# Kernel optimization log

Hardware: AMD Instinct MI355X
Metric: run time of the kernel (lower is better)

## Reference

```python
import math
import jax, jax.numpy as jnp
import numpy as np

# Frozen random shifts from the original module's __init__ (random.randint(-1,1))
SHIFT_C = 1   # p_2_0_1: roll along channel dim
SHIFT_H = 1   # p_4_1_0: roll along h
SHIFT_W = -1  # p_4_1_1: roll along w
K = 7         # horizontal window size (F.unfold kernel (1,7), padding (0,3))


def setup_inputs() -> dict:
    key = jax.random.key(0)
    k1, k2 = jax.random.split(key)
    n, c, h, w = 8, 256, 56, 56
    x = jax.random.normal(k1, (n, c, h, w), dtype=jnp.float32)
    # p_1_w ~ trunc_normal(std=0.1) around 1.0; approximate with 1 + 0.1*normal
    p1w = 1.0 + 0.1 * jax.random.normal(k2, (1, c, h, w), dtype=jnp.float32)
    return {"x": x, "p1w": p1w}


def _unfold_w7(t):
    # t: (n,c,h,w) -> (n,c,7,h,w): 7 horizontal taps, zero-padded (pad=3)
    w = t.shape[-1]
    tp = jnp.pad(t, ((0, 0), (0, 0), (0, 0), (3, 3)))
    return jnp.stack([tp[..., j:j + w] for j in range(K)], axis=2)


def reference(x, p1w):
    n, c, h, w = x.shape
    hw = h * w
    t1 = p1w * x                              # (n,c,h,w)
    t2 = jnp.roll(t1, SHIFT_C, axis=1)        # roll channels
    t3 = _unfold_w7(t2)                       # (n,c,7,h,w)
    t4 = jnp.roll(jnp.roll(t3, SHIFT_H, axis=3), SHIFT_W, axis=4)
    t5 = t1[:, :, None] - t3                  # (n,c,7,h,w)
    t6 = x[:, :, None] + t4                   # (n,c,7,h,w)
    x2 = x.reshape(n, c, hw)
    t5r = t5.reshape(n, c, K, hw)
    t6r = t6.reshape(n, c, K, hw)
    # scores: bmm(x (n,c,hw), t5^T (n,hw,c*7)) -> (n,c,c,7)
    t7 = jnp.einsum('nip,njkp->nijk', x2, t5r) / math.sqrt(hw)
    # aggregate: bmm(t7 (n,c,c*7), t6 (n,c*7,hw)) -> (n,c,hw)
    t8 = jnp.einsum('nijk,njkp->nip', t7, t6r) / math.sqrt(c * K)
    return t8.reshape(n, c, h, w)
```

## Files before the change

kernel.cpp:

```cpp
#include <hip/hip_runtime.h>

typedef unsigned short u16;
typedef unsigned int u32;
typedef unsigned long long u64;
typedef __bf16 bf16x8 __attribute__((ext_vector_type(8)));
typedef float f32x4 __attribute__((ext_vector_type(4)));

#define HH  56
#define WW  56
#define HW  3136
#define CC  256
#define NB  8
#define CKP 2048
#define KS1 4

__device__ __forceinline__ u16 f2bf(float f) {
  unsigned int u = __float_as_uint(f);
  u += 0x7fffu + ((u >> 16) & 1u);
  return (u16)(u >> 16);
}
__device__ __forceinline__ float bf2f(u16 v) {
  return __uint_as_float((unsigned)v << 16);
}

__device__ __forceinline__ void lds_load16(const void* g, void* l) {
  __builtin_amdgcn_global_load_lds(
      (const __attribute__((address_space(1))) void*)g,
      (__attribute__((address_space(3))) void*)l, 16, 0, 0);
}

__global__ void pass1(const float* __restrict__ x, const float* __restrict__ p1w,
                      u16* __restrict__ t1b, u16* __restrict__ xb) {
  const int bi = blockIdx.x;
  const int nb = bi & 7;
  const int inner = bi >> 3;
  const int cw = inner * 256 + threadIdx.x;
  const int i  = nb * (CC * HW / 4) + cw;
  float4 xv = ((const float4*)x)[i];
  float4 wv = ((const float4*)p1w)[cw];
  uint2 xo = make_uint2((unsigned)f2bf(xv.x) | ((unsigned)f2bf(xv.y) << 16),
                        (unsigned)f2bf(xv.z) | ((unsigned)f2bf(xv.w) << 16));
  ((uint2*)xb)[i] = xo;
  uint2 to = make_uint2((unsigned)f2bf(xv.x * wv.x) | ((unsigned)f2bf(xv.y * wv.y) << 16),
                        (unsigned)f2bf(xv.z * wv.z) | ((unsigned)f2bf(xv.w * wv.w) << 16));
  ((uint2*)t1b)[i] = to;
}

__global__ __launch_bounds__(256)
void gemm1f(const u16* __restrict__ A, const u16* __restrict__ t1b,
            float* __restrict__ Cp) {
  __shared__ u16 As[128 * 64];
  __shared__ u16 Bs[128 * 64];

  const int bi = blockIdx.x;
  const int nb = bi & 7;
  const int r  = bi >> 3;
  const int ks = r & 3;
  const int r2 = r >> 2;
  const int m0b = r2 & 1;
  const int n0b = r2 >> 1;

  const int it0 = 49 * ks / KS1, it1 = 49 * (ks + 1) / KS1;
  const u16* Ab  = A   + (long)nb * CC * HW;
  const u16* t1n = t1b + (long)nb * CC * HW;
  const int m0 = m0b * 128, n0 = n0b * 128;
  const int jb = n0b * 16;
  const int t = threadIdx.x;
  const int lane = t & 63, wave = t >> 6;
  const int wm = wave & 1, wn = wave >> 1;
  const int lm = lane & 15, quad = lane >> 4;

  const int jl = (t >> 3) & 15, pc = t & 7, hf = t >> 7;
  const int j  = jb + jl;
  const int jm = (j + CC - 1) & (CC - 1);
  const u16* arow = t1n + (long)j  * HW;
  const u16* wrow = t1n + (long)jm * HW;

  f32x4 acc[4][4];
#pragma unroll
  for (int a = 0; a < 4; ++a)
#pragma unroll
    for (int b = 0; b < 4; ++b) acc[a][b] = (f32x4)0.0f;

  int rowc[4], colc[4];
#pragma unroll
  for (int ci = 0; ci < 4; ++ci) {
    int c = t + ci * 256;
    rowc[ci] = c >> 3;
    colc[ci] = ((c & 7) ^ (rowc[ci] & 7)) * 8;
  }

  for (int it = it0; it < it1; ++it) {
    const int k0 = it * 64;
#pragma unroll
    for (int ci = 0; ci < 4; ++ci)
      lds_load16(Ab + (long)(m0 + rowc[ci]) * HW + k0 + colc[ci],
                 &As[(t + ci * 256) * 8]);

    {
      const int p8 = k0 + pc * 8;
      __attribute__((aligned(16))) u16 Ar[8];
      __attribute__((aligned(16))) u16 Wd[24];
      *(uint4*)Ar = *(const uint4*)&arow[p8];
#pragma unroll
      for (int L = 0; L < 3; ++L) {
        int ad = p8 - 8 + L * 8;
        ad = ad < 0 ? 0 : (ad > HW - 8 ? HW - 8 : ad);
        *(uint4*)&Wd[L * 8] = *(const uint4*)&wrow[ad];
      }
      const int w0t = p8 % 56;
      if (hf == 0) {
#pragma unroll
        for (int k = 0; k < 4; ++k) {
          __attribute__((aligned(16))) u16 v[8];
#pragma unroll
          for (int e = 0; e < 8; ++e)
            v[e] = ((unsigned)(w0t + e + k - 3) < 56u) ? Wd[e + k + 5] : (u16)0;
          *(uint4*)&Bs[(jl * 8 + k) * 64 + (pc ^ k) * 8] = *(const uint4*)v;
        }
      } else {
#pragma unroll
        for (int k = 4; k < 7; ++k) {
          __attribute__((aligned(16))) u16 v[8];
#pragma unroll
          for (int e = 0; e < 8; ++e)
            v[e] = ((unsigned)(w0t + e + k - 3) < 56u) ? Wd[e + k + 5] : (u16)0;
          *(uint4*)&Bs[(jl * 8 + k) * 64 + (pc ^ k) * 8] = *(const uint4*)v;
        }
        *(uint4*)&Bs[(jl * 8 + 7) * 64 + (pc ^ 7) * 8] = *(const uint4*)Ar;
      }
    }
    __syncthreads();
#pragma unroll
    for (int kk = 0; kk < 2; ++kk) {
      const int phys = ((kk * 4 + quad) ^ (lm & 7)) * 8;
      bf16x8 af[4], bv[4];
#pragma unroll
      for (int mi = 0; mi < 4; ++mi)
        af[mi] = *(const bf16x8*)&As[(wm * 64 + mi * 16 + lm) * 64 + phys];
#pragma unroll
      for (int ni = 0; ni < 4; ++ni)
        bv[ni] = *(const bf16x8*)&Bs[(wn * 64 + ni * 16 + lm) * 64 + phys];
#pragma unroll
      for (int mi = 0; mi < 4; ++mi)
#pragma unroll
        for (int ni = 0; ni < 4; ++ni)
          acc[mi][ni] = __builtin_amdgcn_mfma_f32_16x16x32_bf16(
              af[mi], bv[ni], acc[mi][ni], 0, 0, 0);
    }
    __syncthreads();
  }

  float* Cb = Cp + ((long)ks * NB + nb) * (long)CC * CKP;
#pragma unroll
  for (int mi = 0; mi < 4; ++mi)
#pragma unroll
    for (int ni = 0; ni < 4; ++ni) {
      int rb = m0 + wm * 64 + mi * 16 + quad * 4;
      int cg = n0 + wn * 64 + ni * 16 + lm;
#pragma unroll
      for (int r4 = 0; r4 < 4; ++r4)
        Cb[(long)(rb + r4) * CKP + cg] = acc[mi][ni][r4];
    }
}

__global__ void reduce1(const float* __restrict__ p1, u16* __restrict__ t7) {
  const int bi = blockIdx.x;
  const int nb = bi & 7;
  const int gg = (bi >> 3) * 256 + threadIdx.x;
  const long S = (long)NB * CC * CKP;
  const long base = (long)nb * CC * CKP + (long)gg * 8;
  float a[8];
#pragma unroll
  for (int e = 0; e < 8; ++e) a[e] = 0.0f;
#pragma unroll
  for (int ks = 0; ks < KS1; ++ks) {
    float4 lo = *(const float4*)&p1[ks * S + base];
    float4 hi = *(const float4*)&p1[ks * S + base + 4];
    a[0] += lo.x; a[1] += lo.y; a[2] += lo.z; a[3] += lo.w;
    a[4] += hi.x; a[5] += hi.y; a[6] += hi.z; a[7] += hi.w;
  }
  const float s = 1.0f / 56.0f;
  const float G = a[7];
  __attribute__((aligned(16))) u16 o[8];
  float s7 = 0.0f;
#pragma unroll
  for (int k = 0; k < 7; ++k) {
    float v = (G - a[k]) * s;
    s7 += v;
    o[k] = f2bf(v);
  }
  o[7] = f2bf(s7);
  *(uint4*)&t7[base] = *(const uint4*)o;
}

__global__ __launch_bounds__(256)
void gemm2f(const u16* __restrict__ A, const u16* __restrict__ xb,
            const u16* __restrict__ t1b, float* __restrict__ out) {
  __shared__ u16 As0[128 * 64], As1[128 * 64];
  __shared__ u16 Bs[64 * 64];
  __shared__ __attribute__((aligned(16))) u16 Rs0[912], Rs1[912];
  __shared__ __attribute__((aligned(16))) u16 Xs0[512], Xs1[512];

  const int bi = blockIdx.x;
  const int nb = bi & 7;
  const int r  = bi >> 3;
  const int m0b = r & 1;
  const int n0b = r >> 1;

  const u16* Ab  = A   + (long)nb * CC * CKP;
  const u16* xbn = xb  + (long)nb * CC * HW;
  const u16* t1n = t1b + (long)nb * CC * HW;
  const int m0 = m0b * 128, n0 = n0b * 64;
  const int t = threadIdx.x;
  const int lane = t & 63, wave = t >> 6;
  const int wm = wave & 1, wn = wave >> 1;
  const int lm = lane & 15, quad = lane >> 4;

  const int pr = t & 63, jg = t >> 6;
  const int p  = n0 + pr;
  const int h  = p / WW, w = p - h * WW;
  const int w2 = (w + 1) % WW;
  const int swz = pr & 7;
  const int h_lo = n0 / WW;
  const int slot = h - h_lo;

  const int sA   = ((jg * 2 + 0) * 2 + slot) * 56 + w2 - 3;
  const int s4   = sA & ~3;
  const u32 sh   = (u32)(sA & 3) * 16;
  const int b0   = 8 + s4;
  const int b1   = b0 + 112;
  u32 mk01, mk23, mk45, mk6;
  {
    u32 m[7];
#pragma unroll
    for (int k = 0; k < 7; ++k)
      m[k] = ((unsigned)(w2 + k - 3) < 56u) ? 0xffffu : 0u;
    mk01 = m[0] | (m[1] << 16);
    mk23 = m[2] | (m[3] << 16);
    mk45 = m[4] | (m[5] << 16);
    mk6  = m[6];
  }
  const int xoff0 = (jg * 2 + 0) * 64 + pr;
  const int xoff1 = (jg * 2 + 1) * 64 + pr;

  long stSrcOff = 0;
  int  stCh = 0;
  bool stR = false, stX = false;
  {
    if (wave == 1) {
      stX = true; stCh = lane >> 3;
      stSrcOff = n0 + (lane & 7) * 8;
    } else if (wave == 2 || (wave == 3 && lane < 48)) {
      stR = true;
      int c = (wave == 2) ? lane : 64 + lane;
      stCh = c / 14;
      int rem = c - stCh * 14;
      int s = rem / 7, i = rem - s * 7;
      int h2s = ((h_lo + s) + HH - 1) % HH;
      stSrcOff = h2s * 56 + i * 8;
    }
  }

  f32x4 acc[4][2];
#pragma unroll
  for (int a = 0; a < 4; ++a)
#pragma unroll
    for (int b = 0; b < 2; ++b) acc[a][b] = (f32x4)0.0f;

  int rowc[4], colc[4];
#pragma unroll
  for (int ci = 0; ci < 4; ++ci) {
    int c = t + ci * 256;
    rowc[ci] = c >> 3;
    colc[ci] = ((c & 7) ^ (rowc[ci] & 7)) * 8;
  }

#define DMAA(AsD, itn) do { const int k0_ = (itn) * 64;                        \
    _Pragma("unroll")                                                          \
    for (int ci = 0; ci < 4; ++ci)                                             \
      lds_load16(Ab + (long)(m0 + rowc[ci]) * CKP + k0_ + colc[ci],            \
                 &AsD[(t + ci * 256) * 8]); } while (0)

#define STAGE(RsD, XsD, itn) do {                                              \
    if (stX)                                                                   \
      lds_load16(xbn + (long)((itn) * 8 + stCh) * HW + stSrcOff,               \
                 &XsD[lane * 8]);                                              \
    else if (stR) {                                                            \
      const int jmm_ = ((itn) * 8 + stCh + CC - 1) & (CC - 1);                 \
      lds_load16(t1n + (long)jmm_ * HW + stSrcOff,                             \
                 (wave == 2) ? &RsD[8 + lane * 8] : &RsD[8 + 512 + lane * 8]); \
    } } while (0)

#define TAPS(RsS, bofs, xr, d4) do {                                           \
    u64 q0 = *(const u64*)&(RsS)[(bofs)];                                      \
    u64 q1 = *(const u64*)&(RsS)[(bofs) + 4];                                  \
    u64 q2 = *(const u64*)&(RsS)[(bofs) + 8];                                  \
    u64 a_ = (q0 >> sh) | (sh ? (q1 << (64u - sh)) : 0ull);                    \
    u64 b_ = (q1 >> sh) | (sh ? (q2 << (64u - sh)) : 0ull);                    \
    (d4) = make_uint4(((u32)a_) & mk01, ((u32)(a_ >> 32)) & mk23,              \
                      ((u32)b_) & mk45,                                        \
                      (((u32)(b_ >> 32)) & mk6) | ((u32)(xr) << 16));          \
  } while (0)

#define BGEN(RsS, XsS) do {                                                    \
    u16 xr0_ = XsS[xoff0], xr1_ = XsS[xoff1];                                  \
    uint4 d0_, d1_;                                                            \
    TAPS(RsS, b0, xr0_, d0_);                                                  \
    TAPS(RsS, b1, xr1_, d1_);                                                  \
    *(uint4*)&Bs[pr * 64 + (((jg * 2 + 0) ^ swz) * 8)] = d0_;                  \
    *(uint4*)&Bs[pr * 64 + (((jg * 2 + 1) ^ swz) * 8)] = d1_;                  \
  } while (0)

#define MFMA2(AsS) do {                                                        \
    _Pragma("unroll")                                                          \
    for (int kk = 0; kk < 2; ++kk) {                                           \
      const int phys = ((kk * 4 + quad) ^ (lm & 7)) * 8;                       \
      bf16x8 af[4], bv[2];                                                     \
      _Pragma("unroll")                                                        \
      for (int mi = 0; mi < 4; ++mi)                                           \
        af[mi] = *(const bf16x8*)&(AsS)[(wm * 64 + mi * 16 + lm) * 64 + phys]; \
      _Pragma("unroll")                                                        \
      for (int ni = 0; ni < 2; ++ni)                                           \
        bv[ni] = *(const bf16x8*)&Bs[(wn * 32 + ni * 16 + lm) * 64 + phys];    \
      _Pragma("unroll")                                                        \
      for (int mi = 0; mi < 4; ++mi)                                           \
        _Pragma("unroll")                                                      \
        for (int ni = 0; ni < 2; ++ni)                                         \
          acc[mi][ni] = __builtin_amdgcn_mfma_f32_16x16x32_bf16(               \
              af[mi], bv[ni], acc[mi][ni], 0, 0, 0);                           \
    } } while (0)

  STAGE(Rs0, Xs0, 0);
  DMAA(As0, 0);
  __syncthreads();

  for (int itp = 0; itp < 16; ++itp) {
    const int itE = itp * 2;
    BGEN(Rs0, Xs0);
    __syncthreads();
    DMAA(As1, itE + 1);
    STAGE(Rs1, Xs1, itE + 1);
    MFMA2(As0);
    __syncthreads();
    BGEN(Rs1, Xs1);
    __syncthreads();
    if (itE + 2 < 32) {
      DMAA(As0, itE + 2);
      STAGE(Rs0, Xs0, itE + 2);
    }
    MFMA2(As1);
    __syncthreads();
  }

#undef DMAA
#undef STAGE
#undef TAPS
#undef BGEN
#undef MFMA2

  const float s2 = 0.023622783f;
  float* Ob = out + (long)nb * CC * HW;
#pragma unroll
  for (int mi = 0; mi < 4; ++mi)
#pragma unroll
    for (int ni = 0; ni < 2; ++ni) {
      int rb = m0 + wm * 64 + mi * 16 + quad * 4;
      int cg = n0 + wn * 32 + ni * 16 + lm;
#pragma unroll
      for (int r4 = 0; r4 < 4; ++r4)
        Ob[(long)(rb + r4) * HW + cg] = acc[mi][ni][r4] * s2;
    }
}

extern "C" void kernel_launch(void* const* d_in, const int* in_sizes, int n_in,
                              void* d_out, int out_size, void* d_ws, size_t ws_size,
                              hipStream_t stream) {
  const float* x   = (const float*)d_in[0];
  const float* p1w = (const float*)d_in[1];

  char* ws = (char*)d_ws;
  size_t o = 0;
  u16* xb  = (u16*)(ws + o); o += (size_t)NB * CC * HW * 2;
  u16* t1b = (u16*)(ws + o); o += (size_t)NB * CC * HW * 2;
  u16* t7  = (u16*)(ws + o); o += (size_t)NB * CC * CKP * 2;
  float* p1 = (float*)(ws + o); o += (size_t)KS1 * NB * CC * CKP * 4;

  pass1<<<NB * CC * HW / 4 / 256, 256, 0, stream>>>(x, p1w, t1b, xb);
  gemm1f<<<NB * KS1 * 2 * 16, 256, 0, stream>>>(xb, t1b, p1);
  reduce1<<<NB * CC * CKP / 8 / 256, 256, 0, stream>>>(p1, t7);
  gemm2f<<<NB * 2 * 49, 256, 0, stream>>>(t7, xb, t1b, (float*)d_out);
}
```

Baseline: 181.4 us.

## Warp-specialize gemm2f into producer and MFMA consumer waves with double-buffered B

Splits the four waves of gemm2f into two consumer waves that only run MFMAs (each owning a 64x64 output tile with 4x4 accumulators) and two producer waves that stage A via LDS DMA, build the B tile from t1 taps, and prefetch x values straight from global into registers. B is now double-buffered so producers fill the next buffer while consumers compute on the current one, cutting from four barriers per pair of iterations to two. This aims to overlap B-tile generation and loads with MFMA work. In exchange it halves the waves issuing MFMAs, raises per-consumer register pressure, and replaces the LDS-staged x with uncoalesced-ish scalar global loads.

```diff
diff --git a/kernel.cpp b/kernel.cpp
--- a/kernel.cpp
+++ b/kernel.cpp
@@ -198,9 +198,8 @@
 void gemm2f(const u16* __restrict__ A, const u16* __restrict__ xb,
             const u16* __restrict__ t1b, float* __restrict__ out) {
   __shared__ u16 As0[128 * 64], As1[128 * 64];
-  __shared__ u16 Bs[64 * 64];
+  __shared__ u16 Bs0[64 * 64], Bs1[64 * 64];
   __shared__ __attribute__((aligned(16))) u16 Rs0[912], Rs1[912];
-  __shared__ __attribute__((aligned(16))) u16 Xs0[512], Xs1[512];
 
   const int bi = blockIdx.x;
   const int nb = bi & 7;
@@ -214,10 +213,11 @@
   const int m0 = m0b * 128, n0 = n0b * 64;
   const int t = threadIdx.x;
   const int lane = t & 63, wave = t >> 6;
-  const int wm = wave & 1, wn = wave >> 1;
+  const bool consumer = (wave < 2);
   const int lm = lane & 15, quad = lane >> 4;
 
-  const int pr = t & 63, jg = t >> 6;
+  const int pid = t & 127;
+  const int pr = pid & 63, jgrp = pid >> 6;
   const int p  = n0 + pr;
   const int h  = p / WW, w = p - h * WW;
   const int w2 = (w + 1) % WW;
@@ -225,11 +225,10 @@
   const int h_lo = n0 / WW;
   const int slot = h - h_lo;
 
-  const int sA   = ((jg * 2 + 0) * 2 + slot) * 56 + w2 - 3;
-  const int s4   = sA & ~3;
-  const u32 sh   = (u32)(sA & 3) * 16;
-  const int b0   = 8 + s4;
-  const int b1   = b0 + 112;
+  const int sA0  = slot * 56 + w2 - 3;
+  const int s4   = sA0 & ~3;
+  const u32 sh   = (u32)(sA0 & 3) * 16;
+  const int bb   = 8 + s4;
   u32 mk01, mk23, mk45, mk6;
   {
     u32 m[7];
@@ -241,58 +240,52 @@
     mk45 = m[4] | (m[5] << 16);
     mk6  = m[6];
   }
-  const int xoff0 = (jg * 2 + 0) * 64 + pr;
-  const int xoff1 = (jg * 2 + 1) * 64 + pr;
 
   long stSrcOff = 0;
   int  stCh = 0;
-  bool stR = false, stX = false;
-  {
-    if (wave == 1) {
-      stX = true; stCh = lane >> 3;
-      stSrcOff = n0 + (lane & 7) * 8;
-    } else if (wave == 2 || (wave == 3 && lane < 48)) {
-      stR = true;
-      int c = (wave == 2) ? lane : 64 + lane;
-      stCh = c / 14;
-      int rem = c - stCh * 14;
-      int s = rem / 7, i = rem - s * 7;
-      int h2s = ((h_lo + s) + HH - 1) % HH;
-      stSrcOff = h2s * 56 + i * 8;
-    }
-  }
-
-  f32x4 acc[4][2];
-#pragma unroll
-  for (int a = 0; a < 4; ++a)
-#pragma unroll
-    for (int b = 0; b < 2; ++b) acc[a][b] = (f32x4)0.0f;
-
-  int rowc[4], colc[4];
-#pragma unroll
-  for (int ci = 0; ci < 4; ++ci) {
-    int c = t + ci * 256;
+  const bool stR = (!consumer) && (pid < 112);
+  if (stR) {
+    stCh = pid / 14;
+    int rem = pid - stCh * 14;
+    int s = rem / 7, i = rem - s * 7;
+    int h2s = ((h_lo + s) + HH - 1) % HH;
+    stSrcOff = h2s * 56 + i * 8;
+  }
+
+  int rowc[8], colc[8];
+#pragma unroll
+  for (int ci = 0; ci < 8; ++ci) {
+    int c = pid + ci * 128;
     rowc[ci] = c >> 3;
     colc[ci] = ((c & 7) ^ (rowc[ci] & 7)) * 8;
   }
 
+  f32x4 acc[4][4];
+#pragma unroll
+  for (int a = 0; a < 4; ++a)
+#pragma unroll
+    for (int b = 0; b < 4; ++b) acc[a][b] = (f32x4)0.0f;
+
+  u16 xrE[4], xrO[4];
+
 #define DMAA(AsD, itn) do { const int k0_ = (itn) * 64;                        \
     _Pragma("unroll")                                                          \
-    for (int ci = 0; ci < 4; ++ci)                                             \
+    for (int ci = 0; ci < 8; ++ci)                                             \
       lds_load16(Ab + (long)(m0 + rowc[ci]) * CKP + k0_ + colc[ci],            \
-                 &AsD[(t + ci * 256) * 8]); } while (0)
-
-#define STAGE(RsD, XsD, itn) do {                                              \
-    if (stX)                                                                   \
-      lds_load16(xbn + (long)((itn) * 8 + stCh) * HW + stSrcOff,               \
-                 &XsD[lane * 8]);                                              \
-    else if (stR) {                                                            \
-      const int jmm_ = ((itn) * 8 + stCh + CC - 1) & (CC - 1);                 \
-      lds_load16(t1n + (long)jmm_ * HW + stSrcOff,                             \
-                 (wave == 2) ? &RsD[8 + lane * 8] : &RsD[8 + 512 + lane * 8]); \
-    } } while (0)
-
-#define TAPS(RsS, bofs, xr, d4) do {                                           \
+                 &AsD[(pid + ci * 128) * 8]); } while (0)
+
+#define STAGER(RsD, itn) do { if (stR) {                                       \
+    const int jmm_ = ((itn) * 8 + stCh + CC - 1) & (CC - 1);                   \
+    lds_load16(t1n + (long)jmm_ * HW + stSrcOff,                               \
+               (wave == 2) ? &RsD[8 + lane * 8] : &RsD[8 + 512 + lane * 8]);   \
+  } } while (0)
+
+#define XPF(xr, itn) do {                                                      \
+    _Pragma("unroll")                                                          \
+    for (int cc = 0; cc < 4; ++cc)                                             \
+      (xr)[cc] = xbn[(long)((itn) * 8 + jgrp * 4 + cc) * HW + p]; } while (0)
+
+#define TAPS(RsS, bofs, xr1, d4) do {                                          \
     u64 q0 = *(const u64*)&(RsS)[(bofs)];                                      \
     u64 q1 = *(const u64*)&(RsS)[(bofs) + 4];                                  \
     u64 q2 = *(const u64*)&(RsS)[(bofs) + 8];                                  \
@@ -300,77 +293,91 @@
     u64 b_ = (q1 >> sh) | (sh ? (q2 << (64u - sh)) : 0ull);                    \
     (d4) = make_uint4(((u32)a_) & mk01, ((u32)(a_ >> 32)) & mk23,              \
                       ((u32)b_) & mk45,                                        \
-                      (((u32)(b_ >> 32)) & mk6) | ((u32)(xr) << 16));          \
+                      (((u32)(b_ >> 32)) & mk6) | ((u32)(xr1) << 16));         \
   } while (0)
 
-#define BGEN(RsS, XsS) do {                                                    \
-    u16 xr0_ = XsS[xoff0], xr1_ = XsS[xoff1];                                  \
-    uint4 d0_, d1_;                                                            \
-    TAPS(RsS, b0, xr0_, d0_);                                                  \
-    TAPS(RsS, b1, xr1_, d1_);                                                  \
-    *(uint4*)&Bs[pr * 64 + (((jg * 2 + 0) ^ swz) * 8)] = d0_;                  \
-    *(uint4*)&Bs[pr * 64 + (((jg * 2 + 1) ^ swz) * 8)] = d1_;                  \
-  } while (0)
-
-#define MFMA2(AsS) do {                                                        \
+#define BGEN(RsS, xr, BsD) do {                                                \
+    _Pragma("unroll")                                                          \
+    for (int cc = 0; cc < 4; ++cc) {                                           \
+      const int ch_ = jgrp * 4 + cc;                                           \
+      uint4 d_;                                                                \
+      TAPS(RsS, bb + ch_ * 112, (xr)[cc], d_);                                 \
+      *(uint4*)&(BsD)[pr * 64 + ((ch_ ^ swz) * 8)] = d_;                       \
+    } } while (0)
+
+#define MFMAC(AsS, BsS) do {                                                   \
     _Pragma("unroll")                                                          \
     for (int kk = 0; kk < 2; ++kk) {                                           \
       const int phys = ((kk * 4 + quad) ^ (lm & 7)) * 8;                       \
-      bf16x8 af[4], bv[2];                                                     \
+      bf16x8 af[4], bv[4];                                                     \
       _Pragma("unroll")                                                        \
       for (int mi = 0; mi < 4; ++mi)                                           \
-        af[mi] = *(const bf16x8*)&(AsS)[(wm * 64 + mi * 16 + lm) * 64 + phys]; \
+        af[mi] = *(const bf16x8*)&(AsS)[(wave * 64 + mi * 16 + lm) * 64 + phys]; \
       _Pragma("unroll")                                                        \
-      for (int ni = 0; ni < 2; ++ni)                                           \
-        bv[ni] = *(const bf16x8*)&Bs[(wn * 32 + ni * 16 + lm) * 64 + phys];    \
+      for (int ni = 0; ni < 4; ++ni)                                           \
+        bv[ni] = *(const bf16x8*)&(BsS)[(ni * 16 + lm) * 64 + phys];           \
       _Pragma("unroll")                                                        \
       for (int mi = 0; mi < 4; ++mi)                                           \
         _Pragma("unroll")                                                      \
-        for (int ni = 0; ni < 2; ++ni)                                         \
+        for (int ni = 0; ni < 4; ++ni)                                         \
           acc[mi][ni] = __builtin_amdgcn_mfma_f32_16x16x32_bf16(               \
               af[mi], bv[ni], acc[mi][ni], 0, 0, 0);                           \
     } } while (0)
 
-  STAGE(Rs0, Xs0, 0);
-  DMAA(As0, 0);
+  if (!consumer) {
+    STAGER(Rs0, 0);
+    XPF(xrE, 0);
+  }
   __syncthreads();
+  if (!consumer) {
+    BGEN(Rs0, xrE, Bs0);
+    DMAA(As0, 0);
+    STAGER(Rs1, 1);
+    XPF(xrO, 1);
+  }
+  __syncthreads();
 
   for (int itp = 0; itp < 16; ++itp) {
-    const int itE = itp * 2;
-    BGEN(Rs0, Xs0);
+    const int itE = 2 * itp;
+    if (consumer) {
+      MFMAC(As0, Bs0);
+    } else {
+      BGEN(Rs1, xrO, Bs1);
+      DMAA(As1, itE + 1);
+      if (itE + 2 < 32) { STAGER(Rs0, itE + 2); XPF(xrE, itE + 2); }
+    }
     __syncthreads();
-    DMAA(As1, itE + 1);
-    STAGE(Rs1, Xs1, itE + 1);
-    MFMA2(As0);
+    if (consumer) {
+      MFMAC(As1, Bs1);
+    } else if (itE + 2 < 32) {
+      BGEN(Rs0, xrE, Bs0);
+      DMAA(As0, itE + 2);
+      if (itE + 3 < 32) { STAGER(Rs1, itE + 3); XPF(xrO, itE + 3); }
+    }
     __syncthreads();
-    BGEN(Rs1, Xs1);
-    __syncthreads();
-    if (itE + 2 < 32) {
-      DMAA(As0, itE + 2);
-      STAGE(Rs0, Xs0, itE + 2);
-    }
-    MFMA2(As1);
-    __syncthreads();
   }
 
 #undef DMAA
-#undef STAGE
+#undef STAGER
+#undef XPF
 #undef TAPS
 #undef BGEN
-#undef MFMA2
-
-  const float s2 = 0.023622783f;
-  float* Ob = out + (long)nb * CC * HW;
-#pragma unroll
-  for (int mi = 0; mi < 4; ++mi)
-#pragma unroll
-    for (int ni = 0; ni < 2; ++ni) {
-      int rb = m0 + wm * 64 + mi * 16 + quad * 4;
-      int cg = n0 + wn * 32 + ni * 16 + lm;
-#pragma unroll
-      for (int r4 = 0; r4 < 4; ++r4)
-        Ob[(long)(rb + r4) * HW + cg] = acc[mi][ni][r4] * s2;
-    }
+#undef MFMAC
+
+  if (consumer) {
+    const float s2 = 0.023622783f;
+    float* Ob = out + (long)nb * CC * HW;
+#pragma unroll
+    for (int mi = 0; mi < 4; ++mi)
+#pragma unroll
+      for (int ni = 0; ni < 4; ++ni) {
+        int rb = m0 + wave * 64 + mi * 16 + quad * 4;
+        int cg = n0 + ni * 16 + lm;
+#pragma unroll
+        for (int r4 = 0; r4 < 4; ++r4)
+          Ob[(long)(rb + r4) * HW + cg] = acc[mi][ni][r4] * s2;
+      }
+  }
 }
 
 extern "C" void kernel_launch(void* const* d_in, const int* in_sizes, int n_in,
```

After: 197.5 us. 8.9% more time.

## Load GEMM A fragments directly from global into registers, dropping LDS staging

Applied to the files above, without the earlier changes.

The A operand (scores matrix) is no longer copied into double-buffered shared memory. Each lane now loads its MFMA fragments straight from global memory into register double buffers (aE/aO), prefetched one iteration ahead. This removes about 32KB of LDS per block and the LDS read traffic for A, which may raise occupancy. In exchange each wave fetches its own A rows with uncoalesced-ish 16B loads and register pressure goes up; A rows are now re-read from global by both wn wave groups.

```diff
diff --git a/kernel.cpp b/kernel.cpp
--- a/kernel.cpp
+++ b/kernel.cpp
@@ -197,7 +197,6 @@
 __global__ __launch_bounds__(256)
 void gemm2f(const u16* __restrict__ A, const u16* __restrict__ xb,
             const u16* __restrict__ t1b, float* __restrict__ out) {
-  __shared__ u16 As0[128 * 64], As1[128 * 64];
   __shared__ u16 Bs[64 * 64];
   __shared__ __attribute__((aligned(16))) u16 Rs0[912], Rs1[912];
   __shared__ __attribute__((aligned(16))) u16 Xs0[512], Xs1[512];
@@ -216,6 +215,11 @@
   const int lane = t & 63, wave = t >> 6;
   const int wm = wave & 1, wn = wave >> 1;
   const int lm = lane & 15, quad = lane >> 4;
+
+  const u16* aRowP[4];
+#pragma unroll
+  for (int mi = 0; mi < 4; ++mi)
+    aRowP[mi] = Ab + (long)(m0 + wm * 64 + mi * 16 + lm) * CKP + quad * 8;
 
   const int pr = t & 63, jg = t >> 6;
   const int p  = n0 + pr;
@@ -268,19 +272,14 @@
 #pragma unroll
     for (int b = 0; b < 2; ++b) acc[a][b] = (f32x4)0.0f;
 
-  int rowc[4], colc[4];
-#pragma unroll
-  for (int ci = 0; ci < 4; ++ci) {
-    int c = t + ci * 256;
-    rowc[ci] = c >> 3;
-    colc[ci] = ((c & 7) ^ (rowc[ci] & 7)) * 8;
-  }
-
-#define DMAA(AsD, itn) do { const int k0_ = (itn) * 64;                        \
+  bf16x8 aE[8], aO[8];
+
+#define APF(aS, itn) do { const int koff_ = (itn) * 64;                        \
     _Pragma("unroll")                                                          \
-    for (int ci = 0; ci < 4; ++ci)                                             \
-      lds_load16(Ab + (long)(m0 + rowc[ci]) * CKP + k0_ + colc[ci],            \
-                 &AsD[(t + ci * 256) * 8]); } while (0)
+    for (int mi = 0; mi < 4; ++mi) {                                           \
+      (aS)[mi * 2 + 0] = *(const bf16x8*)(aRowP[mi] + koff_);                  \
+      (aS)[mi * 2 + 1] = *(const bf16x8*)(aRowP[mi] + koff_ + 32);             \
+    } } while (0)
 
 #define STAGE(RsD, XsD, itn) do {                                              \
     if (stX)                                                                   \
@@ -312,14 +311,11 @@
     *(uint4*)&Bs[pr * 64 + (((jg * 2 + 1) ^ swz) * 8)] = d1_;                  \
   } while (0)
 
-#define MFMA2(AsS) do {                                                        \
+#define MFMA2R(aS) do {                                                        \
     _Pragma("unroll")                                                          \
     for (int kk = 0; kk < 2; ++kk) {                                           \
       const int phys = ((kk * 4 + quad) ^ (lm & 7)) * 8;                       \
-      bf16x8 af[4], bv[2];                                                     \
-      _Pragma("unroll")                                                        \
-      for (int mi = 0; mi < 4; ++mi)                                           \
-        af[mi] = *(const bf16x8*)&(AsS)[(wm * 64 + mi * 16 + lm) * 64 + phys]; \
+      bf16x8 bv[2];                                                            \
       _Pragma("unroll")                                                        \
       for (int ni = 0; ni < 2; ++ni)                                           \
         bv[ni] = *(const bf16x8*)&Bs[(wn * 32 + ni * 16 + lm) * 64 + phys];    \
@@ -328,36 +324,36 @@
         _Pragma("unroll")                                                      \
         for (int ni = 0; ni < 2; ++ni)                                         \
           acc[mi][ni] = __builtin_amdgcn_mfma_f32_16x16x32_bf16(               \
-              af[mi], bv[ni], acc[mi][ni], 0, 0, 0);                           \
+              (aS)[mi * 2 + kk], bv[ni], acc[mi][ni], 0, 0, 0);                \
     } } while (0)
 
   STAGE(Rs0, Xs0, 0);
-  DMAA(As0, 0);
+  APF(aE, 0);
   __syncthreads();
 
   for (int itp = 0; itp < 16; ++itp) {
     const int itE = itp * 2;
     BGEN(Rs0, Xs0);
     __syncthreads();
-    DMAA(As1, itE + 1);
     STAGE(Rs1, Xs1, itE + 1);
-    MFMA2(As0);
+    APF(aO, itE + 1);
+    MFMA2R(aE);
     __syncthreads();
     BGEN(Rs1, Xs1);
     __syncthreads();
     if (itE + 2 < 32) {
-      DMAA(As0, itE + 2);
       STAGE(Rs0, Xs0, itE + 2);
-    }
-    MFMA2(As1);
-    __syncthreads();
-  }
-
-#undef DMAA
+      APF(aE, itE + 2);
+    }
+    MFMA2R(aO);
+    __syncthreads();
+  }
+
+#undef APF
 #undef STAGE
 #undef TAPS
 #undef BGEN
-#undef MFMA2
+#undef MFMA2R
 
   const float s2 = 0.023622783f;
   float* Ob = out + (long)nb * CC * HW;
```

Result: slower. 259.7 us (+43.1%).
